# Optimization experiments

Measured on AMD Instinct MI355X. Metric: run time of the kernel, lower is better.

## Reference

```python
import jax, jax.numpy as jnp
import numpy as np

N = 10000      # nodes
E = 64000      # edges (includes N self-loops)
IN = 1247      # in_size (text 0:600, audio 600:942, video 942:)
H = 4          # num_heads
D0 = 256       # gcv[1]
D1 = 8         # gcv[2]
OUT = 6        # out_size


def setup_inputs() -> dict:
    key = jax.random.key(0)
    ks = jax.random.split(key, 24)
    s = 0.05
    feats = jax.random.normal(ks[0], (N, IN), jnp.float32)
    drop = jax.random.bernoulli(ks[1], 0.2, (N, IN))
    feats = jnp.where(drop, 0.0, feats)
    # random edges plus self-loops so every node has in-degree >= 1
    src = jnp.concatenate([jax.random.randint(ks[2], (E - N,), 0, N), jnp.arange(N)]).astype(jnp.int32)
    dst = jnp.concatenate([jax.random.randint(ks[3], (E - N,), 0, N), jnp.arange(N)]).astype(jnp.int32)
    textMask = (jnp.zeros(IN).at[:600].set(1.0) * 3.0).astype(jnp.float32)
    audioMask = (jnp.zeros(IN).at[600:942].set(1.0) * 2.0).astype(jnp.float32)
    videoMask = (jnp.zeros(IN).at[942:].set(1.0) * 1.0).astype(jnp.float32)
    return {
        'features': feats, 'src': src, 'dst': dst,
        'textMask': textMask, 'audioMask': audioMask, 'videoMask': videoMask,
        'W2': jax.random.normal(ks[4], (H, IN, D1), jnp.float32) * s,
        'a2': jax.random.normal(ks[5], (H, 2 * D1), jnp.float32) * s,
        'Wl0': jax.random.normal(ks[6], (IN, H * D0), jnp.float32) * s,
        'Wr0': jax.random.normal(ks[7], (IN, H * D0), jnp.float32) * s,
        'a0': jax.random.normal(ks[8], (H, D0), jnp.float32) * s,
        'Wres0': jax.random.normal(ks[9], (IN, H * D0), jnp.float32) * s,
        'b0': jnp.zeros((H * D0,), jnp.float32),
        'Wl1': jax.random.normal(ks[10], (H * D0, H * D1), jnp.float32) * s,
        'Wr1': jax.random.normal(ks[11], (H * D0, H * D1), jnp.float32) * s,
        'a1': jax.random.normal(ks[12], (H, D1), jnp.float32) * s,
        'Wres1': jax.random.normal(ks[13], (H * D0, H * D1), jnp.float32) * s,
        'b1': jnp.zeros((H * D1,), jnp.float32),
        'Wlin': jax.random.normal(ks[14], (2 * H * D1, OUT), jnp.float32) * s,
        'blin': jnp.zeros((OUT,), jnp.float32),
    }


def _segment_softmax(logits, seg, num):
    # logits: [E, H]; softmax over edges sharing the same destination node
    m = jax.ops.segment_max(logits, seg, num_segments=num)
    m = jnp.where(jnp.isfinite(m), m, 0.0)  # guard empty segments
    p = jnp.exp(logits - m[seg])
    denom = jax.ops.segment_sum(p, seg, num_segments=num)
    return p / jnp.maximum(denom[seg], 1e-9)


def _gatv2(x, src, dst, Wl, Wr, attn, Wres, b, h, d, n):
    # DGL GATv2Conv: e = a . leaky_relu(W_l x_u + W_r x_v), edge-softmax over dst,
    # aggregate W_l x_u, add residual projection + bias, relu activation.
    fs = (x @ Wl).reshape(n, h, d)
    fd = (x @ Wr).reshape(n, h, d)
    e = jax.nn.leaky_relu(fs[src] + fd[dst], 0.2)          # [E,H,D]
    logits = jnp.einsum('ehd,hd->eh', e, attn)             # [E,H]
    alpha = _segment_softmax(logits, dst, n)
    out = jax.ops.segment_sum(fs[src] * alpha[..., None], dst, num_segments=n)  # [N,H,D]
    out = out + (x @ Wres).reshape(n, h, d) + b.reshape(h, d)
    return jax.nn.relu(out)


def _gat_inner(x, src, dst, W, a, n):
    # classic multi-head GAT layer (concat merge): e = leaky_relu(a . [z_u || z_v])
    z = jnp.einsum('ni,hio->nho', x, W)                    # [N,H,D1]
    d = z.shape[-1]
    es = jnp.einsum('nho,ho->nh', z, a[:, :d])
    ed = jnp.einsum('nho,ho->nh', z, a[:, d:])
    logits = jax.nn.leaky_relu(es[src] + ed[dst], 0.2)     # [E,H]
    alpha = _segment_softmax(logits, dst, n)
    out = jax.ops.segment_sum(z[src] * alpha[..., None], dst, num_segments=n)
    return out.reshape(n, -1)                              # [N, H*D1]


def reference(features, src, dst, textMask, audioMask, videoMask, W2, a2,
              Wl0, Wr0, a0, Wres0, b0, Wl1, Wr1, a1, Wres1, b1, Wlin, blin):
    h = features
    # mean-impute missing (zero) entries, blend 50/50 with original
    mean = jnp.mean(h, axis=0)
    h1 = jnp.where(h == 0.0, mean[None, :], h)
    h = 0.5 * (h + h1)
    # F.normalize(p=1) per row
    h = h / jnp.maximum(jnp.sum(jnp.abs(h), axis=1, keepdims=True), 1e-12)
    # maskFilter: f*tm + f*am + f*vm
    h = h * (textMask + audioMask + videoMask)
    h3 = _gat_inner(h, src, dst, W2, a2, N)                # [N, 32]
    h = _gatv2(h, src, dst, Wl0, Wr0, a0, Wres0, b0, H, D0, N).reshape(N, -1)
    h = _gatv2(h, src, dst, Wl1, Wr1, a1, Wres1, b1, H, D1, N).reshape(N, -1)
    return jnp.concatenate([h3, h], axis=1) @ Wlin + blin  # [N, OUT]
```

## Files before the change

### kernel.cpp

```cpp
#include <hip/hip_runtime.h>
#include <hip/hip_bf16.h>

#define N_NODES 10000
#define N_EDGES 64000
#define IN_F    1247
#define KPAD    1280
#define NH      4
#define D0      256
#define D1      8
#define HD0     1024
#define HD1     32
#define NBIG    3072
#define NBIG2   3200
#define OUTF    6
#define INV_N   (1.0f / 10000.0f)
#define MPAD    10240

typedef __attribute__((ext_vector_type(8))) short bf16x8;
typedef __attribute__((ext_vector_type(4))) float f32x4;
typedef unsigned int u32;

__device__ __forceinline__ void async_copy16(const unsigned short* gsrc,
                                             unsigned short* ldst) {
    __builtin_amdgcn_global_load_lds(
        (const __attribute__((address_space(1))) u32*)(gsrc),
        (__attribute__((address_space(3))) u32*)(ldst), 16, 0, 0);
}

constexpr size_t OFF_FLAG   = 0;
constexpr size_t OFF_COLSUM = 16;
constexpr size_t OFF_MASKM  = 1296;
constexpr size_t OFF_Z      = 2576;
constexpr size_t OFF_H3     = OFF_Z    + 320000;
constexpr size_t OFF_OUT0   = OFF_H3   + 320000;
constexpr size_t OFF_FS1    = OFF_OUT0 + 10240000;
constexpr size_t OFF_FD1    = OFF_FS1  + 320000;
constexpr size_t OFF_OUT1   = OFF_FD1  + 320000;
constexpr size_t OFF_B0F    = OFF_OUT1 + 320000;
constexpr size_t OFF_B1F    = OFF_B0F  + 1024;
constexpr size_t OFF_DEG    = OFF_B1F  + 64;
constexpr size_t OFF_ROWPTR = OFF_DEG  + 10016;
constexpr size_t OFF_CURSOR = OFF_ROWPTR + 10016;
constexpr size_t OFF_CSRE   = OFF_CURSOR + 10016;
constexpr size_t OFF_FS0B   = OFF_CSRE + 64000;
constexpr size_t OFF_FD0B   = OFF_FS0B + 5120000;
constexpr size_t OFF_ABF    = OFF_FD0B + 5120000;
constexpr size_t OFF_BT     = OFF_ABF  + 6553600;
constexpr size_t OFF_BT1    = OFF_BT   + 2048000;
constexpr size_t WS_FLOATS  = OFF_BT1  + 49152;

__device__ __forceinline__ float ldin(const void* p, size_t i, int f32) {
    return f32 ? ((const float*)p)[i]
               : __bfloat162float(((const __hip_bfloat16*)p)[i]);
}
__device__ __forceinline__ float bfu2f(unsigned short u) {
    union { unsigned int i; float f; } x;
    x.i = ((unsigned int)u) << 16;
    return x.f;
}
__device__ __forceinline__ unsigned short f2bu(float v) {
    __hip_bfloat16 h = __float2bfloat16(v);
    unsigned short u;
    __builtin_memcpy(&u, &h, 2);
    return u;
}


__global__ void init_kernel(const unsigned short* __restrict__ feats_w,
                            int* __restrict__ flag, int* __restrict__ deg,
                            u32* __restrict__ btpad) {
    int b = blockIdx.x, t = threadIdx.x;
    if (b < 64) {
        int found = 0;
        for (int i = b * 256 + t; i < 131072; i += 64 * 256)
            if (((feats_w[i] >> 7) & 0xFF) == 0xFF) found = 1;
        if (found) atomicOr(flag, 1);
    } else if (b < 104) {
        int idx = (b - 64) * 256 + t;
        if (idx < N_NODES + 16) deg[idx] = 0;
    } else {
        int idx = (b - 104) * 256 + t;
        if (idx < 61440) btpad[idx] = 0;
    }
}

__global__ void prepA_kernel(const void* __restrict__ feats, const int* __restrict__ dst,
                             const void* __restrict__ tm, const void* __restrict__ am,
                             const void* __restrict__ vm, const void* __restrict__ b0,
                             const void* __restrict__ b1,
                             float* __restrict__ colsum, int* __restrict__ deg,
                             float* __restrict__ maskmul, float* __restrict__ b0f,
                             float* __restrict__ b1f, const int* __restrict__ dflag) {
    int b = blockIdx.x, t = threadIdx.x;
    if (b < 500) {
        int f32 = *dflag;
        int c = (b % 5) * 256 + t;
        if (c >= IN_F) return;
        int r0 = (b / 5) * 100;
        float s = 0.f;
        for (int r = r0; r < r0 + 100; ++r)
            s += ldin(feats, (size_t)r * IN_F + c, f32);
        atomicAdd(&colsum[c], s);
    } else if (b < 750) {
        int e = (b - 500) * 256 + t;
        if (e < N_EDGES) atomicAdd(&deg[dst[e]], 1);
    } else {
        int f32 = *dflag;
        int c = (b - 750) * 256 + t;
        if (c < IN_F) maskmul[c] = ldin(tm, c, f32) + ldin(am, c, f32) + ldin(vm, c, f32);
        if (c < HD0) b0f[c] = ldin(b0, c, f32);
        if (c < HD1) b1f[c] = ldin(b1, c, f32);
    }
}

__global__ __launch_bounds__(256) void scan_kernel(const int* __restrict__ deg,
                                                   int* __restrict__ rowptr,
                                                   int* __restrict__ cursor) {
    __shared__ int wtot[4];
    int t = threadIdx.x;
    int lane = t & 63, w = t >> 6;
    int base = t * 40;
    int s = 0;
    for (int i = 0; i < 40; ++i) {
        int idx = base + i;
        if (idx < N_NODES) s += deg[idx];
    }
    int inc = s;
#pragma unroll
    for (int d = 1; d < 64; d <<= 1) {
        int v = __shfl_up(inc, d);
        if (lane >= d) inc += v;
    }
    if (lane == 63) wtot[w] = inc;
    __syncthreads();
    int woff = 0;
    for (int ww = 0; ww < w; ++ww) woff += wtot[ww];
    int run = woff + inc - s;
    for (int i = 0; i < 40; ++i) {
        int idx = base + i;
        if (idx < N_NODES) {
            rowptr[idx] = run; cursor[idx] = run;
            run += deg[idx];
        }
    }
    if (t == 255) rowptr[N_NODES] = woff + inc;
}

__global__ void scatter_kernel(const int* __restrict__ dst, int* __restrict__ cursor,
                               int* __restrict__ csr_eid) {
    int e = blockIdx.x * 256 + threadIdx.x;
    if (e >= N_EDGES) return;
    int pos = atomicAdd(&cursor[dst[e]], 1);
    csr_eid[pos] = e;
}

__global__ __launch_bounds__(256) void prepB_kernel(
        const void* __restrict__ feats, const float* __restrict__ colsum,
        const float* __restrict__ maskmul, __hip_bfloat16* __restrict__ abf,
        const void* __restrict__ Wl0, const void* __restrict__ Wr0,
        const void* __restrict__ Wres0, const void* __restrict__ W2,
        __hip_bfloat16* __restrict__ bt,
        const void* __restrict__ Wl1, const void* __restrict__ Wr1,
        const void* __restrict__ Wres1, __hip_bfloat16* __restrict__ bt1,
        const int* __restrict__ dflag) {
    __shared__ float smem[1503];
    int b = blockIdx.x, t = threadIdx.x;
    int f32 = *dflag;
    if (b < MPAD) {
        int n = b;
        unsigned short* arow = (unsigned short*)abf + (size_t)n * KPAD;
        if (n >= N_NODES) {
            if (t < 160) {
                bf16x8 zv = (bf16x8){0, 0, 0, 0, 0, 0, 0, 0};
                *(bf16x8*)(arow + t * 8) = zv;
            }
            return;
        }
        float* rowbuf = smem;
        float* wsum   = smem + 1280;
        float s = 0.f;
        for (int c = t; c < IN_F; c += 256) {
            float f = ldin(feats, (size_t)n * IN_F + c, f32);
            float v = (f != 0.0f) ? f : 0.5f * colsum[c] * INV_N;
            rowbuf[c] = v;
            s += fabsf(v);
        }
#pragma unroll
        for (int off = 32; off > 0; off >>= 1) s += __shfl_xor(s, off);
        if ((t & 63) == 0) wsum[t >> 6] = s;
        __syncthreads();
        float tot = wsum[0] + wsum[1] + wsum[2] + wsum[3];
        float scale = 1.0f / fmaxf(tot, 1e-12f);
        if (t < 160) {
            bf16x8 pv;
#pragma unroll
            for (int j = 0; j < 8; ++j) {
                int k = t * 8 + j;
                float v = (k < IN_F) ? rowbuf[k] * scale * maskmul[k] : 0.f;
                pv[j] = (short)f2bu(v);
            }
            *(bf16x8*)(arow + t * 8) = pv;
        }
    } else if (b < MPAD + 3840) {
        int b2 = b - MPAD;
        int bz = b2 / 1280, rem = b2 - bz * 1280;
        int by = rem >> 5, bx = rem & 31;
        float (*tile)[33] = (float(*)[33])smem;
        int n0 = bx * 32, k0 = by * 32;
        const void* W = (bz == 0) ? Wl0 : (bz == 1) ? Wr0 : Wres0;
        int tx = t & 31, ty = t >> 5;
        for (int i = ty; i < 32; i += 8) {
            int k = k0 + i;
            tile[i][tx] = (k < IN_F) ? ldin(W, (size_t)k * HD0 + n0 + tx, f32) : 0.f;
        }
        __syncthreads();
        for (int i = ty; i < 32; i += 8)
            bt[(size_t)(bz * 1024 + n0 + i) * KPAD + k0 + tx] = __float2bfloat16(tile[tx][i]);
    } else if (b < MPAD + 3840 + 160) {
        int idx = (b - (MPAD + 3840)) * 256 + t;
        if (idx >= 32 * KPAD) return;
        int n = idx / KPAD, k = idx % KPAD;
        int hh = n >> 3, o = n & 7;
        float v = (k < IN_F) ? ldin(W2, ((size_t)hh * IN_F + k) * D1 + o, f32) : 0.f;
        bt[(size_t)(NBIG + n) * KPAD + k] = __float2bfloat16(v);
    } else {
        int idx = (b - (MPAD + 4000)) * 256 + t;
        if (idx >= 96 * HD0) return;
        int n = idx >> 10, k = idx & 1023;
        int seg = n >> 5, col = n & 31;
        const void* W = (seg == 0) ? Wl1 : (seg == 1) ? Wr1 : Wres1;
        bt1[idx] = __float2bfloat16(ldin(W, (size_t)k * HD1 + col, f32));
    }
}

__global__ __launch_bounds__(512) void mfma_gemm(
        const unsigned short* __restrict__ A, const unsigned short* __restrict__ BT,
        const float* __restrict__ b0f, __hip_bfloat16* __restrict__ fs0b,
        __hip_bfloat16* __restrict__ fd0b, __hip_bfloat16* __restrict__ out0r,
        float* __restrict__ z) {
    __shared__ unsigned short As0[8192], Bs0[8192];
    __shared__ unsigned short As1[8192], Bs1[8192];
    __shared__ unsigned short As2[8192], Bs2[8192];
    const int g = blockIdx.x;
    const int xcd = g & 7, l = g >> 3;
    const int colt = l / 5, rowi = l - colt * 5;
    const int bm = (xcd * 5 + rowi) * 256;
    const int bn = colt * 256;
    const int tid = threadIdx.x;
    const int wave = tid >> 6, lane = tid & 63;
    const int quad = lane >> 4, l16 = lane & 15;
    const int wr = wave >> 2, wc = wave & 3;
    const int wm = wr * 128, wn = wc * 64;
    const int srow = lane & 15;
    const int skc  = (lane >> 4) * 8;

    f32x4 acc[8][4];
#pragma unroll
    for (int i = 0; i < 8; ++i)
#pragma unroll
        for (int j = 0; j < 4; ++j) acc[i][j] = (f32x4){0.f, 0.f, 0.f, 0.f};

#define BARX() do { __builtin_amdgcn_s_barrier();                            \
                    __builtin_amdgcn_sched_barrier(0); } while (0)

#define STAGE_A2(kt, dst) do {                                               \
        _Pragma("unroll")                                                    \
        for (int tt = 0; tt < 2; ++tt) {                                     \
            int gg = wave + 8 * tt;                                          \
            async_copy16(A + (size_t)(bm + gg * 16 + srow) * KPAD            \
                             + (kt) + skc,                                   \
                         (dst) + gg * 512);                                  \
        } } while (0)

#define STAGE_B2(kt, dst) do {                                               \
        _Pragma("unroll")                                                    \
        for (int tt = 0; tt < 2; ++tt) {                                     \
            int gg = wave + 8 * tt;                                          \
            int rr = bn + gg * 16 + srow;                                    \
            rr = rr < NBIG2 ? rr : (NBIG2 - 1);                              \
            async_copy16(BT + (size_t)rr * KPAD + (kt) + skc,                \
                         (dst) + gg * 512);                                  \
        } } while (0)

#define LOADAF(buf) do {                                                     \
        _Pragma("unroll")                                                    \
        for (int fb = 0; fb < 8; ++fb)                                       \
            af[fb] = *(const bf16x8*)((buf) + (wr * 8 + fb) * 512            \
                                      + lane * 8);                           \
    } while (0)

#define LOADBF(buf, half) do {                                               \
        _Pragma("unroll")                                                    \
        for (int jj = 0; jj < 2; ++jj)                                       \
            bfr[jj] = *(const bf16x8*)((buf) + (wc * 4 + (half) * 2 + jj)    \
                                       * 512 + lane * 8);                    \
    } while (0)

#define MFMA16(jb) do {                                                      \
        __builtin_amdgcn_s_setprio(1);                                       \
        _Pragma("unroll")                                                    \
        for (int fb = 0; fb < 8; ++fb) {                                     \
            acc[fb][(jb)]     = __builtin_amdgcn_mfma_f32_16x16x32_bf16(     \
                af[fb], bfr[0], acc[fb][(jb)], 0, 0, 0);                     \
            acc[fb][(jb) + 1] = __builtin_amdgcn_mfma_f32_16x16x32_bf16(     \
                af[fb], bfr[1], acc[fb][(jb) + 1], 0, 0, 0);                 \
        }                                                                    \
        __builtin_amdgcn_s_setprio(0);                                       \
    } while (0)

#define KSTEP(curA, curB, preA, preB, kt, dostage, endcnt) do {              \
        bf16x8 af[8], bfr[2];                                                \
        LOADAF(curA);                                                        \
        LOADBF(curB, 0);                                                     \
        if (dostage) STAGE_A2((kt), preA);                                   \
        BARX();                                                              \
        MFMA16(0);                                                           \
        BARX();                                                              \
        LOADBF(curB, 1);                                                     \
        if (dostage) STAGE_B2((kt), preB);                                   \
        BARX();                                                              \
        MFMA16(2);                                                           \
        asm volatile("s_waitcnt vmcnt(" #endcnt ")" ::: "memory");           \
        BARX();                                                              \
    } while (0)

    STAGE_A2(0, As0);  STAGE_B2(0, Bs0);
    STAGE_A2(32, As1); STAGE_B2(32, Bs1);
    asm volatile("s_waitcnt vmcnt(4)" ::: "memory");
    BARX();

    for (int m = 0; m < 36; m += 3) {
        KSTEP(As0, Bs0, As2, Bs2, (m + 2) * 32, 1, 4);
        KSTEP(As1, Bs1, As0, Bs0, (m + 3) * 32, 1, 4);
        KSTEP(As2, Bs2, As1, Bs1, (m + 4) * 32, 1, 4);
    }
    KSTEP(As0, Bs0, As2, Bs2, 38 * 32, 1, 4);
    KSTEP(As1, Bs1, As0, Bs0, 39 * 32, 1, 4);
    KSTEP(As2, Bs2, As0, Bs0, 0,       0, 0);
    KSTEP(As0, Bs0, As1, Bs1, 0,       0, 0);
#undef KSTEP
#undef MFMA16
#undef LOADBF
#undef LOADAF
#undef STAGE_B2
#undef STAGE_A2
#undef BARX

    const int seg = bn >> 10;
#pragma unroll
    for (int i = 0; i < 8; ++i) {
#pragma unroll
        for (int r = 0; r < 4; ++r) {
            int gm = bm + wm + i * 16 + quad * 4 + r;
            if (gm >= N_NODES) continue;
#pragma unroll
            for (int j = 0; j < 4; ++j) {
                int gnl = (bn & 1023) + wn + j * 16 + l16;
                float v = acc[i][j][r];
                if (seg == 0)      fs0b[(size_t)gm * HD0 + gnl] = __float2bfloat16(v);
                else if (seg == 1) fd0b[(size_t)gm * HD0 + gnl] = __float2bfloat16(v);
                else if (seg == 2) out0r[(size_t)gm * HD0 + gnl] = __float2bfloat16(v + b0f[gnl]);
                else if (gnl < HD1) z[(size_t)gm * HD1 + gnl] = v;
            }
        }
    }
}

__global__ __launch_bounds__(256) void att0z_kernel(
        const int* __restrict__ rowptr, const int* __restrict__ csre,
        const int* __restrict__ src, const __hip_bfloat16* __restrict__ fs,
        const __hip_bfloat16* __restrict__ fd, const void* __restrict__ a0,
        const __hip_bfloat16* __restrict__ out0res, __hip_bfloat16* __restrict__ out0b,
        const float* __restrict__ z, const void* __restrict__ a2,
        float* __restrict__ h3, const int* __restrict__ dflag) {
    int f32 = *dflag;
    if (blockIdx.x >= N_NODES) {
        int n = (blockIdx.x - N_NODES) * 8 + (threadIdx.x >> 5);
        int lane = threadIdx.x & 31;
        int h = lane >> 3, o = lane & 7;
        float a2e = ldin(a2, h * 2 * D1 + o, f32);
        float a2d = ldin(a2, h * 2 * D1 + D1 + o, f32);
        float zn = z[(size_t)n * HD1 + lane];
        float edn = zn * a2d;
        edn += __shfl_xor(edn, 1); edn += __shfl_xor(edn, 2); edn += __shfl_xor(edn, 4);
        float den = 0.f, acc = 0.f;
        int start = rowptr[n], end = rowptr[n + 1];
        for (int i = start; i < end; ++i) {
            int s = src[csre[i]];
            float zs = z[(size_t)s * HD1 + lane];
            float esv = zs * a2e;
            esv += __shfl_xor(esv, 1); esv += __shfl_xor(esv, 2); esv += __shfl_xor(esv, 4);
            float x = esv + edn;
            x = x > 0.f ? x : 0.2f * x;
            float p = expf(x);
            den += p;
            acc += p * zs;
        }
        h3[(size_t)n * HD1 + lane] = acc / fmaxf(den, 1e-9f);
        return;
    }
    int n = blockIdx.x;
    int t = threadIdx.x;
    __shared__ float sfd[HD0];
    __shared__ float sa0[HD0];
    __shared__ int sidx[128];
    int start = rowptr[n], end = rowptr[n + 1];
    int deg = end - start;
    {
        const unsigned short* fdp = (const unsigned short*)fd + (size_t)n * HD0;
        ushort4 u = *(const ushort4*)(fdp + 4 * t);
        sfd[4 * t + 0] = bfu2f(u.x); sfd[4 * t + 1] = bfu2f(u.y);
        sfd[4 * t + 2] = bfu2f(u.z); sfd[4 * t + 3] = bfu2f(u.w);
#pragma unroll
        for (int i = 0; i < 4; ++i) sa0[4 * t + i] = ldin(a0, 4 * t + i, f32);
        if (t < deg && t < 128) sidx[t] = src[csre[start + t]];
    }
    __syncthreads();
    const unsigned short* fsu = (const unsigned short*)fs;
    float den = 0.f;
    float acc[4] = {0.f, 0.f, 0.f, 0.f};
#pragma unroll 2
    for (int i = 0; i < deg; ++i) {
        int s = (i < 128) ? sidx[i] : src[csre[start + i]];
        ushort4 u = *(const ushort4*)(fsu + (size_t)s * HD0 + 4 * t);
        float fv[4], part = 0.f;
#pragma unroll
        for (int j = 0; j < 4; ++j) {
            unsigned short uj = (j == 0) ? u.x : (j == 1) ? u.y : (j == 2) ? u.z : u.w;
            fv[j] = bfu2f(uj);
            float x = fv[j] + sfd[4 * t + j];
            x = x > 0.f ? x : 0.2f * x;
            part += x * sa0[4 * t + j];
        }
        for (int off = 32; off > 0; off >>= 1) part += __shfl_xor(part, off);
        float p = expf(part);
        den += p;
#pragma unroll
        for (int j = 0; j < 4; ++j) acc[j] += p * fv[j];
    }
    float inv = 1.0f / fmaxf(den, 1e-9f);
    ushort4 ub = *(const ushort4*)((const unsigned short*)out0res + (size_t)n * HD0 + 4 * t);
    ushort4 o;
    o.x = f2bu(fmaxf(bfu2f(ub.x) + acc[0] * inv, 0.f));
    o.y = f2bu(fmaxf(bfu2f(ub.y) + acc[1] * inv, 0.f));
    o.z = f2bu(fmaxf(bfu2f(ub.z) + acc[2] * inv, 0.f));
    o.w = f2bu(fmaxf(bfu2f(ub.w) + acc[3] * inv, 0.f));
    *(ushort4*)((unsigned short*)out0b + (size_t)n * HD0 + 4 * t) = o;
}

__global__ __launch_bounds__(256) void mfma_gemm96(
        const unsigned short* __restrict__ A, const unsigned short* __restrict__ BT1,
        const float* __restrict__ b1f, float* __restrict__ fs1,
        float* __restrict__ fd1, float* __restrict__ out1,
        float* __restrict__ fs1b, float* __restrict__ fd1b,
        float* __restrict__ out1b) {
    __shared__ unsigned short As0[2048], Bs0[3072], As1[2048], Bs1[3072];
    const int tid = threadIdx.x;
    const int wave = tid >> 6, lane = tid & 63;
    const int quad = lane >> 4, l16 = lane & 15;
    const int bk = blockIdx.x >= 157;
    const int bm = (blockIdx.x - (bk ? 157 : 0)) * 64;
    const int kbase = bk ? 512 : 0;
    const int srow = lane & 15;
    const int skc  = (lane >> 4) * 8;
    const int NIT = 512 / 32;

    f32x4 acc[6];
#pragma unroll
    for (int j = 0; j < 6; ++j) acc[j] = (f32x4){0.f, 0.f, 0.f, 0.f};

#define STAGE96(kk, Adst, Bdst) do {                                              \
        async_copy16(A + (size_t)(bm + wave * 16 + srow) * HD0 + kbase + (kk) + skc, \
                     (Adst) + wave * 512);                                        \
        async_copy16(BT1 + (size_t)(wave * 16 + srow) * HD0 + kbase + (kk) + skc, \
                     (Bdst) + wave * 512);                                        \
        if (wave < 2)                                                             \
            async_copy16(BT1 + (size_t)((4 + wave) * 16 + srow) * HD0 + kbase + (kk) + skc, \
                         (Bdst) + (4 + wave) * 512);                              \
        } while (0)

#define COMPUTE96(Asrc, Bsrc) do {                                                \
        bf16x8 af = *(const bf16x8*)((Asrc) + wave * 512 + lane * 8);             \
        _Pragma("unroll")                                                         \
        for (int j = 0; j < 6; ++j) {                                             \
            bf16x8 bfr = *(const bf16x8*)((Bsrc) + j * 512 + lane * 8);           \
            acc[j] = __builtin_amdgcn_mfma_f32_16x16x32_bf16(af, bfr, acc[j], 0, 0, 0); \
        } } while (0)

    STAGE96(0, As0, Bs0);
    for (int it = 0; it < NIT; it += 2) {
        asm volatile("s_waitcnt vmcnt(0)" ::: "memory");
        asm volatile("s_barrier" ::: "memory");
        STAGE96((it + 1) * 32, As1, Bs1);
        COMPUTE96(As0, Bs0);
        asm volatile("s_waitcnt vmcnt(0)" ::: "memory");
        asm volatile("s_barrier" ::: "memory");
        if (it + 2 < NIT) STAGE96((it + 2) * 32, As0, Bs0);
        COMPUTE96(As1, Bs1);
    }
#undef STAGE96
#undef COMPUTE96

#pragma unroll
    for (int r = 0; r < 4; ++r) {
        int gm = bm + wave * 16 + quad * 4 + r;
        if (gm >= N_NODES) continue;
#pragma unroll
        for (int j = 0; j < 6; ++j) {
            int col = j * 16 + l16;
            int seg = col >> 5, cl = col & 31;
            float v = acc[j][r];
            if (!bk) {
                if (seg == 0)      fs1[(size_t)gm * HD1 + cl] = v;
                else if (seg == 1) fd1[(size_t)gm * HD1 + cl] = v;
                else               out1[(size_t)gm * HD1 + cl] = v + b1f[cl];
            } else {
                if (seg == 0)      fs1b[(size_t)gm * HD1 + cl] = v;
                else if (seg == 1) fd1b[(size_t)gm * HD1 + cl] = v;
                else               out1b[(size_t)gm * HD1 + cl] = v;
            }
        }
    }
}

__global__ __launch_bounds__(256) void att32e_final_kernel(
        const int* __restrict__ rowptr, const int* __restrict__ csre,
        const int* __restrict__ src, const float* __restrict__ fs1,
        const float* __restrict__ fd1, const void* __restrict__ a1,
        const float* __restrict__ out1g, const float* __restrict__ h3,
        const void* __restrict__ Wlin, const void* __restrict__ blin,
        void* __restrict__ out, const int* __restrict__ dflag,
        const float* __restrict__ fs1b, const float* __restrict__ fd1b,
        const float* __restrict__ out1gb) {
    int f32 = *dflag;
    int n = blockIdx.x * 8 + (threadIdx.x >> 5);
    int lane = threadIdx.x & 31;
    size_t ni = (size_t)n * HD1 + lane;
    float fdn = fd1[ni] + fd1b[ni];
    float a = ldin(a1, lane, f32);
    float den = 0.f, acc = 0.f;
    int start = rowptr[n], end = rowptr[n + 1];
    for (int i = start; i < end; ++i) {
        int s = src[csre[i]];
        size_t si = (size_t)s * HD1 + lane;
        float fsv = fs1[si] + fs1b[si];
        float x = fsv + fdn;
        x = x > 0.f ? x : 0.2f * x;
        float term = x * a;
        term += __shfl_xor(term, 1);
        term += __shfl_xor(term, 2);
        term += __shfl_xor(term, 4);
        float p = expf(term);
        den += p;
        acc += p * fsv;
    }
    float out1v = fmaxf(out1g[ni] + out1gb[ni] + acc / fmaxf(den, 1e-9f), 0.f);
    float h3v = h3[ni];
    float partial[OUTF];
#pragma unroll
    for (int o = 0; o < OUTF; ++o)
        partial[o] = h3v * ldin(Wlin, (size_t)lane * OUTF + o, f32)
                   + out1v * ldin(Wlin, (size_t)(HD1 + lane) * OUTF + o, f32);
#pragma unroll
    for (int st = 1; st <= 16; st <<= 1)
#pragma unroll
        for (int o = 0; o < OUTF; ++o) partial[o] += __shfl_xor(partial[o], st);
    if (lane == 0) {
#pragma unroll
        for (int o = 0; o < OUTF; ++o) {
            float v = partial[o] + ldin(blin, o, f32);
            if (f32) ((float*)out)[(size_t)n * OUTF + o] = v;
            else     ((__hip_bfloat16*)out)[(size_t)n * OUTF + o] = __float2bfloat16(v);
        }
    }
}

extern "C" void kernel_launch(void* const* d_in, const int* in_sizes, int n_in,
                              void* d_out, int out_size, void* d_ws, size_t ws_size,
                              hipStream_t stream) {
    const void* feats = d_in[0];
    const int*  src   = (const int*)d_in[1];
    const int*  dst   = (const int*)d_in[2];
    const void* tm    = d_in[3];
    const void* am    = d_in[4];
    const void* vm    = d_in[5];
    const void* W2    = d_in[6];
    const void* a2    = d_in[7];
    const void* Wl0   = d_in[8];
    const void* Wr0   = d_in[9];
    const void* a0    = d_in[10];
    const void* Wres0 = d_in[11];
    const void* b0    = d_in[12];
    const void* Wl1   = d_in[13];
    const void* Wr1   = d_in[14];
    const void* a1    = d_in[15];
    const void* Wres1 = d_in[16];
    const void* b1    = d_in[17];
    const void* Wlin  = d_in[18];
    const void* blin  = d_in[19];

    float* ws = (float*)d_ws;
    int*   dflag  = (int*)(ws + OFF_FLAG);
    float* colsum = ws + OFF_COLSUM;
    float* maskm  = ws + OFF_MASKM;
    float* z      = ws + OFF_Z;
    float* h3     = ws + OFF_H3;
    float* fs1    = ws + OFF_FS1;
    float* fd1    = ws + OFF_FD1;
    float* out1   = ws + OFF_OUT1;
    float* b0f    = ws + OFF_B0F;
    float* b1f    = ws + OFF_B1F;
    int*   deg    = (int*)(ws + OFF_DEG);
    int*   rowptr = (int*)(ws + OFF_ROWPTR);
    int*   cursor = (int*)(ws + OFF_CURSOR);
    int*   csre   = (int*)(ws + OFF_CSRE);
    __hip_bfloat16* out0r = (__hip_bfloat16*)(ws + OFF_OUT0);
    __hip_bfloat16* fs0b = (__hip_bfloat16*)(ws + OFF_FS0B);
    __hip_bfloat16* fd0b = (__hip_bfloat16*)(ws + OFF_FD0B);
    __hip_bfloat16* abf  = (__hip_bfloat16*)(ws + OFF_ABF);
    __hip_bfloat16* bt   = (__hip_bfloat16*)(ws + OFF_BT);
    __hip_bfloat16* bt1  = (__hip_bfloat16*)(ws + OFF_BT1);
    __hip_bfloat16* out0b = fd0b;
    float* fs1b  = ws + OFF_ABF;
    float* fd1b  = ws + OFF_ABF + 320000;
    float* out1b = ws + OFF_ABF + 640000;

    (void)hipMemsetAsync(ws, 0, (16 + 1280) * sizeof(float), stream);

    init_kernel<<<344, 256, 0, stream>>>((const unsigned short*)feats, dflag, deg,
                                         (u32*)(bt + (size_t)(NBIG + HD1) * KPAD));
    prepA_kernel<<<755, 256, 0, stream>>>(feats, dst, tm, am, vm, b0, b1,
                                          colsum, deg, maskm, b0f, b1f, dflag);
    scan_kernel<<<1, 256, 0, stream>>>(deg, rowptr, cursor);
    scatter_kernel<<<(N_EDGES + 255) / 256, 256, 0, stream>>>(dst, cursor, csre);

    prepB_kernel<<<MPAD + 3840 + 160 + 384, 256, 0, stream>>>(
        feats, colsum, maskm, abf, Wl0, Wr0, Wres0, W2, bt, Wl1, Wr1, Wres1, bt1, dflag);

    mfma_gemm<<<520, 512, 0, stream>>>(
        (const unsigned short*)abf, (const unsigned short*)bt, b0f, fs0b, fd0b, out0r, z);

    att0z_kernel<<<N_NODES + N_NODES / 8, 256, 0, stream>>>(
        rowptr, csre, src, fs0b, fd0b, a0, out0r, out0b, z, a2, h3, dflag);

    mfma_gemm96<<<314, 256, 0, stream>>>(
        (const unsigned short*)out0b, (const unsigned short*)bt1, b1f,
        fs1, fd1, out1, fs1b, fd1b, out1b);

    att32e_final_kernel<<<N_NODES / 8, 256, 0, stream>>>(
        rowptr, csre, src, fs1, fd1, a1, out1, h3, Wlin, blin, d_out, dflag,
        fs1b, fd1b, out1b);
}
```

Baseline: 502.6 us.

## Process one row per wave in prep and fold GEMM tail tiles into fewer blocks

The row-normalisation part of prepB now gives each wave one node row, keeping values in registers and reducing with shuffles. This removes the shared-memory buffer and the block-wide barrier and cuts the block count by four. The main GEMM grid shrinks from 520 to 512 blocks, and the first block of each XCD computes an extra tail tile (tile index 64) in a loop. This removes a partial second wave of blocks but makes those eight blocks do twice the work. The bf16 row stores become scalar per-lane writes instead of 16-byte vector stores.

```diff
diff --git a/kernel.cpp b/kernel.cpp
--- a/kernel.cpp
+++ b/kernel.cpp
@@ -163,46 +163,40 @@
         const void* __restrict__ Wl1, const void* __restrict__ Wr1,
         const void* __restrict__ Wres1, __hip_bfloat16* __restrict__ bt1,
         const int* __restrict__ dflag) {
-    __shared__ float smem[1503];
+    __shared__ float smem[1056];
     int b = blockIdx.x, t = threadIdx.x;
     int f32 = *dflag;
-    if (b < MPAD) {
-        int n = b;
+    if (b < 2560) {
+        int w = t >> 6, lane = t & 63;
+        int n = b * 4 + w;
         unsigned short* arow = (unsigned short*)abf + (size_t)n * KPAD;
         if (n >= N_NODES) {
-            if (t < 160) {
-                bf16x8 zv = (bf16x8){0, 0, 0, 0, 0, 0, 0, 0};
-                *(bf16x8*)(arow + t * 8) = zv;
-            }
+#pragma unroll
+            for (int j = 0; j < 20; ++j) arow[j * 64 + lane] = 0;
             return;
         }
-        float* rowbuf = smem;
-        float* wsum   = smem + 1280;
+        float v[20];
         float s = 0.f;
-        for (int c = t; c < IN_F; c += 256) {
-            float f = ldin(feats, (size_t)n * IN_F + c, f32);
-            float v = (f != 0.0f) ? f : 0.5f * colsum[c] * INV_N;
-            rowbuf[c] = v;
-            s += fabsf(v);
+#pragma unroll
+        for (int j = 0; j < 20; ++j) {
+            int c = j * 64 + lane;
+            float f = (c < IN_F) ? ldin(feats, (size_t)n * IN_F + c, f32) : 0.f;
+            float vv = (f != 0.0f) ? f
+                     : ((c < IN_F) ? 0.5f * colsum[c] * INV_N : 0.f);
+            v[j] = vv;
+            s += fabsf(vv);
         }
 #pragma unroll
         for (int off = 32; off > 0; off >>= 1) s += __shfl_xor(s, off);
-        if ((t & 63) == 0) wsum[t >> 6] = s;
-        __syncthreads();
-        float tot = wsum[0] + wsum[1] + wsum[2] + wsum[3];
-        float scale = 1.0f / fmaxf(tot, 1e-12f);
-        if (t < 160) {
-            bf16x8 pv;
-#pragma unroll
-            for (int j = 0; j < 8; ++j) {
-                int k = t * 8 + j;
-                float v = (k < IN_F) ? rowbuf[k] * scale * maskmul[k] : 0.f;
-                pv[j] = (short)f2bu(v);
-            }
-            *(bf16x8*)(arow + t * 8) = pv;
-        }
-    } else if (b < MPAD + 3840) {
-        int b2 = b - MPAD;
+        float scale = 1.0f / fmaxf(s, 1e-12f);
+#pragma unroll
+        for (int j = 0; j < 20; ++j) {
+            int c = j * 64 + lane;
+            float vv = (c < IN_F) ? v[j] * scale * maskmul[c] : 0.f;
+            arow[c] = f2bu(vv);
+        }
+    } else if (b < 2560 + 3840) {
+        int b2 = b - 2560;
         int bz = b2 / 1280, rem = b2 - bz * 1280;
         int by = rem >> 5, bx = rem & 31;
         float (*tile)[33] = (float(*)[33])smem;
@@ -216,15 +210,15 @@
         __syncthreads();
         for (int i = ty; i < 32; i += 8)
             bt[(size_t)(bz * 1024 + n0 + i) * KPAD + k0 + tx] = __float2bfloat16(tile[tx][i]);
-    } else if (b < MPAD + 3840 + 160) {
-        int idx = (b - (MPAD + 3840)) * 256 + t;
+    } else if (b < 2560 + 3840 + 160) {
+        int idx = (b - (2560 + 3840)) * 256 + t;
         if (idx >= 32 * KPAD) return;
         int n = idx / KPAD, k = idx % KPAD;
         int hh = n >> 3, o = n & 7;
         float v = (k < IN_F) ? ldin(W2, ((size_t)hh * IN_F + k) * D1 + o, f32) : 0.f;
         bt[(size_t)(NBIG + n) * KPAD + k] = __float2bfloat16(v);
     } else {
-        int idx = (b - (MPAD + 4000)) * 256 + t;
+        int idx = (b - (2560 + 4000)) * 256 + t;
         if (idx >= 96 * HD0) return;
         int n = idx >> 10, k = idx & 1023;
         int seg = n >> 5, col = n & 31;
@@ -242,10 +236,8 @@
     __shared__ unsigned short As1[8192], Bs1[8192];
     __shared__ unsigned short As2[8192], Bs2[8192];
     const int g = blockIdx.x;
-    const int xcd = g & 7, l = g >> 3;
-    const int colt = l / 5, rowi = l - colt * 5;
-    const int bm = (xcd * 5 + rowi) * 256;
-    const int bn = colt * 256;
+    const int xcd = g & 7, jloc = g >> 3;
+    const int nrep = (jloc == 0) ? 2 : 1;
     const int tid = threadIdx.x;
     const int wave = tid >> 6, lane = tid & 63;
     const int quad = lane >> 4, l16 = lane & 15;
@@ -253,12 +245,6 @@
     const int wm = wr * 128, wn = wc * 64;
     const int srow = lane & 15;
     const int skc  = (lane >> 4) * 8;
-
-    f32x4 acc[8][4];
-#pragma unroll
-    for (int i = 0; i < 8; ++i)
-#pragma unroll
-        for (int j = 0; j < 4; ++j) acc[i][j] = (f32x4){0.f, 0.f, 0.f, 0.f};
 
 #define BARX() do { __builtin_amdgcn_s_barrier();                            \
                     __builtin_amdgcn_sched_barrier(0); } while (0)
@@ -324,20 +310,52 @@
         BARX();                                                              \
     } while (0)
 
-    STAGE_A2(0, As0);  STAGE_B2(0, Bs0);
-    STAGE_A2(32, As1); STAGE_B2(32, Bs1);
-    asm volatile("s_waitcnt vmcnt(4)" ::: "memory");
-    BARX();
-
-    for (int m = 0; m < 36; m += 3) {
-        KSTEP(As0, Bs0, As2, Bs2, (m + 2) * 32, 1, 4);
-        KSTEP(As1, Bs1, As0, Bs0, (m + 3) * 32, 1, 4);
-        KSTEP(As2, Bs2, As1, Bs1, (m + 4) * 32, 1, 4);
-    }
-    KSTEP(As0, Bs0, As2, Bs2, 38 * 32, 1, 4);
-    KSTEP(As1, Bs1, As0, Bs0, 39 * 32, 1, 4);
-    KSTEP(As2, Bs2, As0, Bs0, 0,       0, 0);
-    KSTEP(As0, Bs0, As1, Bs1, 0,       0, 0);
+    for (int rep = 0; rep < nrep; ++rep) {
+        const int l = (rep == 0) ? jloc : 64;
+        const int colt = l / 5, rowi = l - colt * 5;
+        const int bm = (xcd * 5 + rowi) * 256;
+        const int bn = colt * 256;
+
+        f32x4 acc[8][4];
+#pragma unroll
+        for (int i = 0; i < 8; ++i)
+#pragma unroll
+            for (int j = 0; j < 4; ++j) acc[i][j] = (f32x4){0.f, 0.f, 0.f, 0.f};
+
+        STAGE_A2(0, As0);  STAGE_B2(0, Bs0);
+        STAGE_A2(32, As1); STAGE_B2(32, Bs1);
+        asm volatile("s_waitcnt vmcnt(4)" ::: "memory");
+        BARX();
+
+        for (int m = 0; m < 36; m += 3) {
+            KSTEP(As0, Bs0, As2, Bs2, (m + 2) * 32, 1, 4);
+            KSTEP(As1, Bs1, As0, Bs0, (m + 3) * 32, 1, 4);
+            KSTEP(As2, Bs2, As1, Bs1, (m + 4) * 32, 1, 4);
+        }
+        KSTEP(As0, Bs0, As2, Bs2, 38 * 32, 1, 4);
+        KSTEP(As1, Bs1, As0, Bs0, 39 * 32, 1, 4);
+        KSTEP(As2, Bs2, As0, Bs0, 0,       0, 0);
+        KSTEP(As0, Bs0, As1, Bs1, 0,       0, 0);
+
+        const int seg = bn >> 10;
+#pragma unroll
+        for (int i = 0; i < 8; ++i) {
+#pragma unroll
+            for (int r = 0; r < 4; ++r) {
+                int gm = bm + wm + i * 16 + quad * 4 + r;
+                if (gm >= N_NODES) continue;
+#pragma unroll
+                for (int j = 0; j < 4; ++j) {
+                    int gnl = (bn & 1023) + wn + j * 16 + l16;
+                    float v = acc[i][j][r];
+                    if (seg == 0)      fs0b[(size_t)gm * HD0 + gnl] = __float2bfloat16(v);
+                    else if (seg == 1) fd0b[(size_t)gm * HD0 + gnl] = __float2bfloat16(v);
+                    else if (seg == 2) out0r[(size_t)gm * HD0 + gnl] = __float2bfloat16(v + b0f[gnl]);
+                    else if (gnl < HD1) z[(size_t)gm * HD1 + gnl] = v;
+                }
+            }
+        }
+    }
 #undef KSTEP
 #undef MFMA16
 #undef LOADBF
@@ -345,25 +363,6 @@
 #undef STAGE_B2
 #undef STAGE_A2
 #undef BARX
-
-    const int seg = bn >> 10;
-#pragma unroll
-    for (int i = 0; i < 8; ++i) {
-#pragma unroll
-        for (int r = 0; r < 4; ++r) {
-            int gm = bm + wm + i * 16 + quad * 4 + r;
-            if (gm >= N_NODES) continue;
-#pragma unroll
-            for (int j = 0; j < 4; ++j) {
-                int gnl = (bn & 1023) + wn + j * 16 + l16;
-                float v = acc[i][j][r];
-                if (seg == 0)      fs0b[(size_t)gm * HD0 + gnl] = __float2bfloat16(v);
-                else if (seg == 1) fd0b[(size_t)gm * HD0 + gnl] = __float2bfloat16(v);
-                else if (seg == 2) out0r[(size_t)gm * HD0 + gnl] = __float2bfloat16(v + b0f[gnl]);
-                else if (gnl < HD1) z[(size_t)gm * HD1 + gnl] = v;
-            }
-        }
-    }
 }
 
 __global__ __launch_bounds__(256) void att0z_kernel(
@@ -634,10 +633,10 @@
     scan_kernel<<<1, 256, 0, stream>>>(deg, rowptr, cursor);
     scatter_kernel<<<(N_EDGES + 255) / 256, 256, 0, stream>>>(dst, cursor, csre);
 
-    prepB_kernel<<<MPAD + 3840 + 160 + 384, 256, 0, stream>>>(
+    prepB_kernel<<<2560 + 3840 + 160 + 384, 256, 0, stream>>>(
         feats, colsum, maskm, abf, Wl0, Wr0, Wres0, W2, bt, Wl1, Wr1, Wres1, bt1, dflag);
 
-    mfma_gemm<<<520, 512, 0, stream>>>(
+    mfma_gemm<<<512, 512, 0, stream>>>(
         (const unsigned short*)abf, (const unsigned short*)bt, b0f, fs0b, fd0b, out0r, z);
 
     att0z_kernel<<<N_NODES + N_NODES / 8, 256, 0, stream>>>(
```

Result: faster. 492.3 us (-2.0%).
